# Kernel optimization log

Measured on AMD Instinct MI355X. Metric: run time of the kernel, lower is better.

Reference implementation:

```python
import jax, jax.numpy as jnp
import numpy as np

B, C, H, W = 16, 16, 256, 256
HID, OUT_C, IN_C = 128, 13, 3

_SOBEL_X = np.array([[-1, 0, 1], [-2, 0, 2], [-1, 0, 1]], dtype=np.float32)
_SOBEL_Y = _SOBEL_X.T


def setup_inputs() -> dict:
    key = jax.random.key(0)
    k1, k2, k3, k4 = jax.random.split(key, 4)
    return {
        "input_grid": jax.random.normal(k1, (B, C, H, W), dtype=jnp.float32),
        "w1": jax.random.normal(k2, (HID, 3 * C), dtype=jnp.float32) * 0.0001,
        "b1": jax.random.normal(k3, (HID,), dtype=jnp.float32) * 0.0001,
        "w2": jax.random.normal(k4, (OUT_C, HID), dtype=jnp.float32) * 0.0001,
    }


def _depthwise_sobel(x_padded, filt2d):
    # x_padded: [B, C, H+2, W+2]; depthwise 3x3 valid conv (groups=C)
    c = x_padded.shape[1]
    kern = jnp.broadcast_to(jnp.asarray(filt2d)[None, None], (c, 1, 3, 3))
    return jax.lax.conv_general_dilated(
        x_padded, kern, window_strides=(1, 1), padding="VALID",
        feature_group_count=c,
        dimension_numbers=("NCHW", "OIHW", "NCHW"))


def reference(input_grid, w1, b1, w2):
    # circular pad by 1 on spatial dims
    xp = jnp.pad(input_grid, ((0, 0), (0, 0), (1, 1), (1, 1)), mode="wrap")
    gx = _depthwise_sobel(xp, _SOBEL_X)
    gy = _depthwise_sobel(xp, _SOBEL_Y)
    # perception grid: [B, 3C, H, W]
    perception = jnp.concatenate([input_grid, gx, gy], axis=1)
    # update network: 1x1 conv -> ReLU -> 1x1 conv (dropout = identity in eval)
    h = jax.nn.relu(jnp.einsum("bchw,oc->bohw", perception, w1)
                    + b1[None, :, None, None])
    ds = jnp.einsum("bchw,oc->bohw", h, w2)  # [B, C-IN_C, H, W]
    # residual add to channels 3: of the state
    return input_grid.at[:, IN_C:].add(ds)
```

## Files before the change

### kernel.cpp

```cpp
#include <hip/hip_runtime.h>

#define BB   16
#define CC   16
#define HH   256
#define WW   256
#define HID  128
#define OUTC 13

typedef short short8 __attribute__((ext_vector_type(8)));
typedef float floatx16 __attribute__((ext_vector_type(16)));

__device__ __forceinline__ unsigned short f2bf(float x) {
    unsigned int u = __float_as_uint(x);
    u += 0x7fffu + ((u >> 16) & 1u);
    return (unsigned short)(u >> 16);
}

#define W2F_OFF   36864

__global__ __launch_bounds__(256) void gca_prep(
    const float* __restrict__ w1, const float* __restrict__ w2,
    unsigned char* __restrict__ ws)
{
    const int id = blockIdx.x * 256 + threadIdx.x;
    const float SX[9] = {-1.f, 0.f, 1.f, -2.f, 0.f, 2.f, -1.f, 0.f, 1.f};
    const float SY[9] = {-1.f, -2.f, -1.f, 0.f, 0.f, 0.f, 1.f, 2.f, 1.f};

    if (id < 2304) {
        const int mtG  = id / 576;
        const int rem  = id % 576;
        const int tap  = rem / 64;
        const int lane = rem % 64;
        const int p  = lane & 31, hi = lane >> 5;
        const int hid = 32 * mtG + p;
        const float cen = (tap == 4) ? 1.f : 0.f;
        const float sxv = SX[tap], syv = SY[tap];
        const float* wr = w1 + hid * 48;
        unsigned int o[4];
        for (int k = 0; k < 4; ++k) {
            int c0 = 8 * hi + 2 * k;
            float v0 = wr[c0]     * cen + wr[16 + c0]     * sxv + wr[32 + c0]     * syv;
            float v1 = wr[c0 + 1] * cen + wr[16 + c0 + 1] * sxv + wr[32 + c0 + 1] * syv;
            o[k] = (unsigned int)f2bf(v0) | ((unsigned int)f2bf(v1) << 16);
        }
        *(uint4*)(ws + (size_t)id * 16) = make_uint4(o[0], o[1], o[2], o[3]);
    } else if (id < 2816) {
        const int id2 = id - 2304;
        const int s    = id2 / 64;
        const int lane = id2 % 64;
        const int outc = lane & 31, hi = lane >> 5;
        unsigned int o[4];
        for (int k = 0; k < 4; ++k) {
            int hid0 = 16 * s + 8 * hi + 2 * k;
            float v0 = (outc < OUTC) ? w2[outc * HID + hid0]     : 0.f;
            float v1 = (outc < OUTC) ? w2[outc * HID + hid0 + 1] : 0.f;
            o[k] = (unsigned int)f2bf(v0) | ((unsigned int)f2bf(v1) << 16);
        }
        *(uint4*)(ws + W2F_OFF + (size_t)id2 * 16) = make_uint4(o[0], o[1], o[2], o[3]);
    }
}

#define TILE_DW 3400

__global__ __launch_bounds__(256) void gca_main(
    const float* __restrict__ in,
    const float* __restrict__ b1,
    const unsigned char* __restrict__ ws,
    float* __restrict__ out)
{
    __shared__ unsigned int lds[TILE_DW];

    const int tid  = threadIdx.x;
    const int wid  = tid >> 6;
    const int lane = tid & 63;
    const int p    = lane & 31;
    const int hi   = lane >> 5;

    const int bI = blockIdx.x >> 8;
    const int rm = blockIdx.x & 255;
    const int y0 = (rm >> 3) << 3;
    const int x0 = (rm & 7)  << 5;

    {
        unsigned short* tus = (unsigned short*)lds;
        const float* inb = in + ((size_t)bI << 20);
        for (int i = tid; i < 16 * 10 * 34; i += 256) {
            int col = i % 34;
            int rem = i / 34;
            int row = rem % 10;
            int c   = rem / 10;
            int y = (y0 + row - 1) & 255;
            int x = (x0 + col - 1) & 255;
            float v = inb[(c << 16) + (y << 8) + x];
            tus[(row * 34 + col) * 20 + c] = f2bf(v);
        }
    }
    __syncthreads();

#pragma unroll 1
    for (int rr2 = 0; rr2 < 2; ++rr2) {
        const int r   = 2 * wid + rr2;
        const int row = y0 + r;

        floatx16 acc1[4];
#pragma unroll
        for (int mt = 0; mt < 4; ++mt)
#pragma unroll
            for (int q = 0; q < 4; ++q) {
                float4 bv = *(const float4*)(b1 + 32 * mt + 8 * q + 4 * hi);
                acc1[mt][4 * q + 0] = bv.x;
                acc1[mt][4 * q + 1] = bv.y;
                acc1[mt][4 * q + 2] = bv.z;
                acc1[mt][4 * q + 3] = bv.w;
            }

#pragma unroll
        for (int tap = 0; tap < 9; ++tap) {
            const int tr  = r + tap / 3;
            const int col = p + tap % 3;
            const int dwo = (tr * 34 + col) * 10 + 4 * hi;
            union { unsigned int u[4]; short8 s; } bfr;
            uint2 lo2 = *(const uint2*)&lds[dwo];
            uint2 hi2 = *(const uint2*)&lds[dwo + 2];
            bfr.u[0] = lo2.x; bfr.u[1] = lo2.y; bfr.u[2] = hi2.x; bfr.u[3] = hi2.y;
#pragma unroll
            for (int mt = 0; mt < 4; ++mt) {
                short8 af = *(const short8*)(ws + (size_t)((mt * 9 + tap) * 64 + lane) * 16);
                acc1[mt] = __builtin_amdgcn_mfma_f32_32x32x16_bf16(af, bfr.s, acc1[mt], 0, 0, 0);
            }
        }

        uint2 hrun[16];
#pragma unroll
        for (int mt = 0; mt < 4; ++mt)
#pragma unroll
            for (int q = 0; q < 4; ++q) {
                float h0 = fmaxf(acc1[mt][4 * q + 0], 0.f);
                float h1 = fmaxf(acc1[mt][4 * q + 1], 0.f);
                float h2 = fmaxf(acc1[mt][4 * q + 2], 0.f);
                float h3 = fmaxf(acc1[mt][4 * q + 3], 0.f);
                hrun[4 * mt + q].x = (unsigned int)f2bf(h0) | ((unsigned int)f2bf(h1) << 16);
                hrun[4 * mt + q].y = (unsigned int)f2bf(h2) | ((unsigned int)f2bf(h3) << 16);
            }

        floatx16 acc2 = {};
#pragma unroll
        for (int s = 0; s < 8; ++s) {
            uint2 r0 = hrun[2 * s];
            uint2 r1 = hrun[2 * s + 1];
            uint2 x0s, x1s;
            x0s.x = (unsigned int)__shfl_xor((int)r0.x, 32);
            x0s.y = (unsigned int)__shfl_xor((int)r0.y, 32);
            x1s.x = (unsigned int)__shfl_xor((int)r1.x, 32);
            x1s.y = (unsigned int)__shfl_xor((int)r1.y, 32);
            union { unsigned int u[4]; short8 s8; } b2;
            uint2 lo = hi ? x1s : r0;
            uint2 hg = hi ? r1  : x0s;
            b2.u[0] = lo.x; b2.u[1] = lo.y; b2.u[2] = hg.x; b2.u[3] = hg.y;
            short8 a2 = *(const short8*)(ws + W2F_OFF + (size_t)(s * 64 + lane) * 16);
            acc2 = __builtin_amdgcn_mfma_f32_32x32x16_bf16(a2, b2.s8, acc2, 0, 0, 0);
        }

#pragma unroll
        for (int reg = 0; reg < 16; ++reg) {
            int oc = (reg & 3) + 8 * (reg >> 2) + 4 * hi;
            if (oc < OUTC) {
                int idx = ((bI * 16 + 3 + oc) << 16) + (row << 8) + x0 + p;
                out[idx] = in[idx] + acc2[reg];
            }
        }
        {
            int c  = lane >> 5;
            int idx = ((bI * 16 + c) << 16) + (row << 8) + x0 + p;
            out[idx] = in[idx];
            if (lane < 32) {
                int idx2 = ((bI * 16 + 2) << 16) + (row << 8) + x0 + lane;
                out[idx2] = in[idx2];
            }
        }
    }
}

extern "C" void kernel_launch(void* const* d_in, const int* in_sizes, int n_in,
                              void* d_out, int out_size, void* d_ws, size_t ws_size,
                              hipStream_t stream) {
    const float* x  = (const float*)d_in[0];
    const float* w1 = (const float*)d_in[1];
    const float* b1 = (const float*)d_in[2];
    const float* w2 = (const float*)d_in[3];
    float* out = (float*)d_out;
    unsigned char* ws = (unsigned char*)d_ws;

    hipLaunchKernelGGL(gca_prep, dim3(11), dim3(256), 0, stream, w1, w2, ws);
    hipLaunchKernelGGL(gca_main, dim3(4096), dim3(256), 0, stream, x, b1, ws, out);
}
```

Before: 260.5 us.

## Stage W1 fragments in LDS, double tile height, split hidden loop for registers

```diff
diff --git a/kernel.cpp b/kernel.cpp
--- a/kernel.cpp
+++ b/kernel.cpp
@@ -60,15 +60,17 @@
     }
 }
 
-#define TILE_DW 3400
-
-__global__ __launch_bounds__(256) void gca_main(
+#define TILE_DW 6120
+#define W1L_DW  9216
+#define LDS_DW  (TILE_DW + W1L_DW)
+
+__global__ __launch_bounds__(512, 4) void gca_main(
     const float* __restrict__ in,
     const float* __restrict__ b1,
     const unsigned char* __restrict__ ws,
     float* __restrict__ out)
 {
-    __shared__ unsigned int lds[TILE_DW];
+    __shared__ unsigned int lds[LDS_DW];
 
     const int tid  = threadIdx.x;
     const int wid  = tid >> 6;
@@ -76,19 +78,24 @@
     const int p    = lane & 31;
     const int hi   = lane >> 5;
 
-    const int bI = blockIdx.x >> 8;
-    const int rm = blockIdx.x & 255;
-    const int y0 = (rm >> 3) << 3;
+    const int bI = blockIdx.x >> 7;
+    const int rm = blockIdx.x & 127;
+    const int y0 = (rm >> 3) << 4;
     const int x0 = (rm & 7)  << 5;
+
+    for (int i = tid; i < 2304; i += 512) {
+        uint4 v = ((const uint4*)ws)[i];
+        *(uint4*)&lds[TILE_DW + 4 * i] = v;
+    }
 
     {
         unsigned short* tus = (unsigned short*)lds;
         const float* inb = in + ((size_t)bI << 20);
-        for (int i = tid; i < 16 * 10 * 34; i += 256) {
-            int col = i % 34;
-            int rem = i / 34;
-            int row = rem % 10;
-            int c   = rem / 10;
+        for (int i = tid; i < 16 * 18 * 34; i += 512) {
+            int c   = i / 612;
+            int rem = i % 612;
+            int row = rem / 34;
+            int col = rem % 34;
             int y = (y0 + row - 1) & 255;
             int x = (x0 + col - 1) & 255;
             float v = inb[(c << 16) + (y << 8) + x];
@@ -102,63 +109,68 @@
         const int r   = 2 * wid + rr2;
         const int row = y0 + r;
 
-        floatx16 acc1[4];
-#pragma unroll
-        for (int mt = 0; mt < 4; ++mt)
-#pragma unroll
-            for (int q = 0; q < 4; ++q) {
-                float4 bv = *(const float4*)(b1 + 32 * mt + 8 * q + 4 * hi);
-                acc1[mt][4 * q + 0] = bv.x;
-                acc1[mt][4 * q + 1] = bv.y;
-                acc1[mt][4 * q + 2] = bv.z;
-                acc1[mt][4 * q + 3] = bv.w;
-            }
-
-#pragma unroll
-        for (int tap = 0; tap < 9; ++tap) {
-            const int tr  = r + tap / 3;
-            const int col = p + tap % 3;
-            const int dwo = (tr * 34 + col) * 10 + 4 * hi;
-            union { unsigned int u[4]; short8 s; } bfr;
-            uint2 lo2 = *(const uint2*)&lds[dwo];
-            uint2 hi2 = *(const uint2*)&lds[dwo + 2];
-            bfr.u[0] = lo2.x; bfr.u[1] = lo2.y; bfr.u[2] = hi2.x; bfr.u[3] = hi2.y;
-#pragma unroll
-            for (int mt = 0; mt < 4; ++mt) {
-                short8 af = *(const short8*)(ws + (size_t)((mt * 9 + tap) * 64 + lane) * 16);
-                acc1[mt] = __builtin_amdgcn_mfma_f32_32x32x16_bf16(af, bfr.s, acc1[mt], 0, 0, 0);
-            }
-        }
-
-        uint2 hrun[16];
-#pragma unroll
-        for (int mt = 0; mt < 4; ++mt)
-#pragma unroll
-            for (int q = 0; q < 4; ++q) {
-                float h0 = fmaxf(acc1[mt][4 * q + 0], 0.f);
-                float h1 = fmaxf(acc1[mt][4 * q + 1], 0.f);
-                float h2 = fmaxf(acc1[mt][4 * q + 2], 0.f);
-                float h3 = fmaxf(acc1[mt][4 * q + 3], 0.f);
-                hrun[4 * mt + q].x = (unsigned int)f2bf(h0) | ((unsigned int)f2bf(h1) << 16);
-                hrun[4 * mt + q].y = (unsigned int)f2bf(h2) | ((unsigned int)f2bf(h3) << 16);
-            }
-
         floatx16 acc2 = {};
-#pragma unroll
-        for (int s = 0; s < 8; ++s) {
-            uint2 r0 = hrun[2 * s];
-            uint2 r1 = hrun[2 * s + 1];
-            uint2 x0s, x1s;
-            x0s.x = (unsigned int)__shfl_xor((int)r0.x, 32);
-            x0s.y = (unsigned int)__shfl_xor((int)r0.y, 32);
-            x1s.x = (unsigned int)__shfl_xor((int)r1.x, 32);
-            x1s.y = (unsigned int)__shfl_xor((int)r1.y, 32);
-            union { unsigned int u[4]; short8 s8; } b2;
-            uint2 lo = hi ? x1s : r0;
-            uint2 hg = hi ? r1  : x0s;
-            b2.u[0] = lo.x; b2.u[1] = lo.y; b2.u[2] = hg.x; b2.u[3] = hg.y;
-            short8 a2 = *(const short8*)(ws + W2F_OFF + (size_t)(s * 64 + lane) * 16);
-            acc2 = __builtin_amdgcn_mfma_f32_32x32x16_bf16(a2, b2.s8, acc2, 0, 0, 0);
+
+#pragma unroll
+        for (int pg = 0; pg < 2; ++pg) {
+            floatx16 acc1[2];
+#pragma unroll
+            for (int m = 0; m < 2; ++m)
+#pragma unroll
+                for (int q = 0; q < 4; ++q) {
+                    float4 bv = *(const float4*)(b1 + 64 * pg + 32 * m + 8 * q + 4 * hi);
+                    acc1[m][4 * q + 0] = bv.x;
+                    acc1[m][4 * q + 1] = bv.y;
+                    acc1[m][4 * q + 2] = bv.z;
+                    acc1[m][4 * q + 3] = bv.w;
+                }
+
+#pragma unroll
+            for (int tap = 0; tap < 9; ++tap) {
+                const int tr  = r + tap / 3;
+                const int col = p + tap % 3;
+                const int dwo = (tr * 34 + col) * 10 + 4 * hi;
+                union { unsigned int u[4]; short8 s; } bfr;
+                uint2 lo2 = *(const uint2*)&lds[dwo];
+                uint2 hi2 = *(const uint2*)&lds[dwo + 2];
+                bfr.u[0] = lo2.x; bfr.u[1] = lo2.y; bfr.u[2] = hi2.x; bfr.u[3] = hi2.y;
+#pragma unroll
+                for (int m = 0; m < 2; ++m) {
+                    const int mt = 2 * pg + m;
+                    short8 af = *(const short8*)&lds[TILE_DW + 4 * ((mt * 9 + tap) * 64 + lane)];
+                    acc1[m] = __builtin_amdgcn_mfma_f32_32x32x16_bf16(af, bfr.s, acc1[m], 0, 0, 0);
+                }
+            }
+
+            uint2 hrun[8];
+#pragma unroll
+            for (int m = 0; m < 2; ++m)
+#pragma unroll
+                for (int q = 0; q < 4; ++q) {
+                    float h0 = fmaxf(acc1[m][4 * q + 0], 0.f);
+                    float h1 = fmaxf(acc1[m][4 * q + 1], 0.f);
+                    float h2 = fmaxf(acc1[m][4 * q + 2], 0.f);
+                    float h3 = fmaxf(acc1[m][4 * q + 3], 0.f);
+                    hrun[4 * m + q].x = (unsigned int)f2bf(h0) | ((unsigned int)f2bf(h1) << 16);
+                    hrun[4 * m + q].y = (unsigned int)f2bf(h2) | ((unsigned int)f2bf(h3) << 16);
+                }
+
+#pragma unroll
+            for (int sp = 0; sp < 4; ++sp) {
+                uint2 r0 = hrun[2 * sp];
+                uint2 r1 = hrun[2 * sp + 1];
+                uint2 x0s, x1s;
+                x0s.x = (unsigned int)__shfl_xor((int)r0.x, 32);
+                x0s.y = (unsigned int)__shfl_xor((int)r0.y, 32);
+                x1s.x = (unsigned int)__shfl_xor((int)r1.x, 32);
+                x1s.y = (unsigned int)__shfl_xor((int)r1.y, 32);
+                union { unsigned int u[4]; short8 s8; } b2;
+                uint2 lo = hi ? x1s : r0;
+                uint2 hg = hi ? r1  : x0s;
+                b2.u[0] = lo.x; b2.u[1] = lo.y; b2.u[2] = hg.x; b2.u[3] = hg.y;
+                short8 a2 = *(const short8*)(ws + W2F_OFF + (size_t)((4 * pg + sp) * 64 + lane) * 16);
+                acc2 = __builtin_amdgcn_mfma_f32_32x32x16_bf16(a2, b2.s8, acc2, 0, 0, 0);
+            }
         }
 
 #pragma unroll
@@ -192,5 +204,5 @@
     unsigned char* ws = (unsigned char*)d_ws;
 
     hipLaunchKernelGGL(gca_prep, dim3(11), dim3(256), 0, stream, w1, w2, ws);
-    hipLaunchKernelGGL(gca_main, dim3(4096), dim3(256), 0, stream, x, b1, ws, out);
-}
+    hipLaunchKernelGGL(gca_main, dim3(2048), dim3(512), 0, stream, x, b1, ws, out);
+}
```

New measurement: 694.8 us. 2.67x slower.
